# Performance work log

Measured on AMD Instinct MI355X. Metric: run time of the kernel, lower is better.

The kernel has to match this reference:

```python
import jax, jax.numpy as jnp
import numpy as np

B, IN, OUT = 8192, 4096, 4096

def setup_inputs() -> dict:
    key = jax.random.key(0)
    k1, k2, k3 = jax.random.split(key, 3)
    x = jax.random.normal(k1, (B, IN), dtype=jnp.float32)
    # nn.Linear default init: U(-1/sqrt(in), 1/sqrt(in))
    bound = 1.0 / np.sqrt(IN)
    W = jax.random.uniform(k2, (OUT, IN), dtype=jnp.float32, minval=-bound, maxval=bound)
    b = jax.random.uniform(k3, (OUT,), dtype=jnp.float32, minval=-bound, maxval=bound)
    return {"x": x, "W": W, "b": b}

def reference(x, W, b):
    # L2-normalize each row (eps added to norm, matching torch)
    norm = jnp.sqrt(jnp.sum(x * x, axis=1, keepdims=True))
    x_n = x / (norm + 1e-8)
    # Linear: y = x_n @ W^T + b, then ReLU
    y = jnp.einsum('bi,oi->bo', x_n, W) + b
    return jax.nn.relu(y)
```

## Files before the change

### kernel.cpp

```cpp
#include <hip/hip_runtime.h>
#include <hip/hip_bf16.h>
#include <cstdint>
#include <cstddef>

#define GLB(p)  ((const __attribute__((address_space(1))) void*)(p))
#define LDSP(p) ((__attribute__((address_space(3))) void*)(p))

typedef __attribute__((ext_vector_type(8))) __bf16 bf16x8;
typedef __attribute__((ext_vector_type(4))) float  f32x4;
typedef __attribute__((ext_vector_type(8))) unsigned short u16x8;

static constexpr int Mdim = 8192, Ndim = 4096, Kdim = 4096;

#define S_BAR()      do { asm volatile("" ::: "memory"); __builtin_amdgcn_s_barrier(); asm volatile("" ::: "memory"); } while (0)
#define WAIT_LGKM(n) asm volatile("s_waitcnt lgkmcnt(" #n ")" ::: "memory")
#define WAIT_VM(n)   asm volatile("s_waitcnt vmcnt(" #n ")" ::: "memory")

static __device__ __forceinline__ unsigned short f2bf_bits(float f) {
    __hip_bfloat16 h = __float2bfloat16(f);
    return __builtin_bit_cast(unsigned short, h);
}

static __device__ __forceinline__ int swz16k(int p) {
    return p ^ (((p >> 7) & 7) << 4);
}

__global__ void __launch_bounds__(256) preproc_kernel(const float* __restrict__ x,
                                                      const float* __restrict__ Wf,
                                                      __hip_bfloat16* __restrict__ xn,
                                                      __hip_bfloat16* __restrict__ Wb)
{
    const int row = blockIdx.x;
    const int t = threadIdx.x;

    const float4* xr = (const float4*)(x + (size_t)row * Kdim);
    float4 v[4];
    float s = 0.f;
#pragma unroll
    for (int i = 0; i < 4; ++i) {
        v[i] = xr[i * 256 + t];
        s += v[i].x * v[i].x + v[i].y * v[i].y + v[i].z * v[i].z + v[i].w * v[i].w;
    }
#pragma unroll
    for (int off = 32; off > 0; off >>= 1) s += __shfl_down(s, off, 64);
    __shared__ float red[4];
    const int lane = t & 63, w = t >> 6;
    if (lane == 0) red[w] = s;
    __syncthreads();
    const float tot = red[0] + red[1] + red[2] + red[3];
    const float inv = 1.f / (sqrtf(tot) + 1e-8f);
    ushort4* xo = (ushort4*)(xn + (size_t)row * Kdim);
#pragma unroll
    for (int i = 0; i < 4; ++i) {
        ushort4 o;
        o.x = f2bf_bits(v[i].x * inv);
        o.y = f2bf_bits(v[i].y * inv);
        o.z = f2bf_bits(v[i].z * inv);
        o.w = f2bf_bits(v[i].w * inv);
        xo[i * 256 + t] = o;
    }

    const size_t idx = (size_t)row * 256 + t;
    const float4* p = (const float4*)Wf + idx * 2;
    const float4 a = p[0], c = p[1];
    u16x8 o;
    o[0] = f2bf_bits(a.x); o[1] = f2bf_bits(a.y);
    o[2] = f2bf_bits(a.z); o[3] = f2bf_bits(a.w);
    o[4] = f2bf_bits(c.x); o[5] = f2bf_bits(c.y);
    o[6] = f2bf_bits(c.z); o[7] = f2bf_bits(c.w);
    *((u16x8*)Wb + idx) = o;
}

__global__ void __launch_bounds__(512, 2) gemm256_8p(
        const __hip_bfloat16* __restrict__ A,
        const __hip_bfloat16* __restrict__ B,
        const float* __restrict__ bias,
        float* __restrict__ out)
{
    constexpr int NT  = Kdim / 64;
    constexpr int NTN = Ndim / 256;
    constexpr int NWG = (Mdim / 256) * NTN;
    extern __shared__ char smem[];

    const int bid = blockIdx.x;
    const int swz = (bid & 7) * (NWG / 8) + (bid >> 3);
    const int m0 = (swz / NTN) * 256;
    const int n0 = (swz % NTN) * 256;

    const int tid  = threadIdx.x;
    const int lane = tid & 63;
    const int w    = tid >> 6;
    const int wm   = w >> 2;
    const int wn   = w & 3;
    const int fr   = lane & 15;
    const int ko2  = (lane >> 4) * 16;
    const int xm   = (lane & 7) << 4;
    const int brow = (wn & 1) * 64;

    const int p0 = tid * 16;
    const int p1 = 8192 + tid * 16;
    const int q0 = swz16k(p0);
    const int q1 = swz16k(p1);
    const int sr0 = q0 >> 7, sc0 = (q0 & 127) >> 1;
    const int sr1 = q1 >> 7, sc1 = (q1 & 127) >> 1;

    const __hip_bfloat16* Ab0 = A + (size_t)(m0 + sr0) * Kdim + sc0;
    const __hip_bfloat16* Ab1 = A + (size_t)(m0 + sr1) * Kdim + sc1;
    const __hip_bfloat16* Bb0 = B + (size_t)(n0 + sr0) * Kdim + sc0;
    const __hip_bfloat16* Bb1 = B + (size_t)(n0 + sr1) * Kdim + sc1;

#define STAGE_A(tt, h) do { \
        char* ld_ = smem + ((2 * (tt) + (h)) & 3) * 16384; \
        __builtin_amdgcn_global_load_lds(GLB(Ab0 + (size_t)(h) * (128 * Kdim) + (tt) * 64), LDSP(ld_ + p0), 16, 0, 0); \
        __builtin_amdgcn_global_load_lds(GLB(Ab1 + (size_t)(h) * (128 * Kdim) + (tt) * 64), LDSP(ld_ + p1), 16, 0, 0); \
    } while (0)
#define STAGE_B(tt, h) do { \
        char* ld_ = smem + 65536 + ((2 * (tt) + (h)) & 3) * 16384; \
        __builtin_amdgcn_global_load_lds(GLB(Bb0 + (size_t)(h) * (128 * Kdim) + (tt) * 64), LDSP(ld_ + p0), 16, 0, 0); \
        __builtin_amdgcn_global_load_lds(GLB(Bb1 + (size_t)(h) * (128 * Kdim) + (tt) * 64), LDSP(ld_ + p1), 16, 0, 0); \
    } while (0)

#define LDS_RD(base, row, kb) (*(const bf16x8*)(smem + ((((base) + (row) * 128 + (kb))) ^ xm)))

#define A_READS(mb) do { \
    _Pragma("unroll") for (int i = 0; i < 2; ++i) { \
        afr[i][0] = LDS_RD(sa, ((mb) + i) * 16 + fr, ko2); \
        afr[i][1] = LDS_RD(sa, ((mb) + i) * 16 + fr, 64 + ko2); } } while (0)

#define MFMA_PHASE(mb) do { \
    __builtin_amdgcn_s_setprio(1); \
    _Pragma("unroll") for (int kk = 0; kk < 2; ++kk) \
    _Pragma("unroll") for (int i = 0; i < 2; ++i) \
    _Pragma("unroll") for (int j = 0; j < 4; ++j) \
        acc[(mb) + i][j] = __builtin_amdgcn_mfma_f32_16x16x32_bf16(afr[i][kk], bfr[j][kk], acc[(mb) + i][j], 0, 0, 0); \
    __builtin_amdgcn_s_setprio(0); } while (0)

    f32x4 acc[8][4];
#pragma unroll
    for (int i = 0; i < 8; ++i)
#pragma unroll
        for (int j = 0; j < 4; ++j) acc[i][j] = (f32x4){0.f, 0.f, 0.f, 0.f};

    bf16x8 afr[2][2], bfr[4][2];

    STAGE_A(0, 0); STAGE_A(0, 1); STAGE_B(0, 0); STAGE_B(0, 1);
    STAGE_A(1, 0); STAGE_A(1, 1);
    WAIT_VM(4);
    S_BAR();

#pragma unroll 2
    for (int t = 0; t < NT; ++t) {
        const int sa = ((2 * t + wm) & 3) * 16384;
        const int sb = 65536 + ((2 * t + (wn >> 1)) & 3) * 16384;
        const int tb = (t + 1) & (NT - 1);
        const int ta = (t + 2) & (NT - 1);

#pragma unroll
        for (int j = 0; j < 4; ++j) {
            bfr[j][0] = LDS_RD(sb, brow + j * 16 + fr, ko2);
            bfr[j][1] = LDS_RD(sb, brow + j * 16 + fr, 64 + ko2);
        }
        A_READS(0);
        STAGE_B(tb, 0); STAGE_B(tb, 1);
        MFMA_PHASE(0);

        A_READS(2);
        MFMA_PHASE(2);

        A_READS(4);
        MFMA_PHASE(4);

        A_READS(6);
        WAIT_LGKM(0);
        S_BAR();
        STAGE_A(ta, 0); STAGE_A(ta, 1);
        MFMA_PHASE(6);
        WAIT_VM(4);
        S_BAR();
    }
    WAIT_VM(0);

#undef STAGE_A
#undef STAGE_B
#undef LDS_RD
#undef A_READS
#undef MFMA_PHASE

    const int cl = lane & 15;
    const int rl = (lane >> 4) * 4;
#pragma unroll
    for (int j = 0; j < 4; ++j) {
        const int col = n0 + wn * 64 + j * 16 + cl;
        const float bv = bias[col];
#pragma unroll
        for (int i = 0; i < 8; ++i) {
            const int row = m0 + wm * 128 + i * 16 + rl;
            float* po = out + (size_t)row * Ndim + col;
#pragma unroll
            for (int q = 0; q < 4; ++q) {
                const float r = acc[i][j][q] + bv;
                po[(size_t)q * Ndim] = r > 0.f ? r : 0.f;
            }
        }
    }
}

__global__ void __launch_bounds__(256) gemm_bias_relu_kernel(
        const __hip_bfloat16* __restrict__ A,
        const __hip_bfloat16* __restrict__ B,
        const float* __restrict__ bias,
        float* __restrict__ out)
{
    constexpr int BM = 128, BN = 128, BK = 32;
    constexpr int NT_N = Ndim / BN;
    constexpr int NWG  = (Mdim / BM) * NT_N;

    __shared__ __bf16 As[BM * BK];
    __shared__ __bf16 Bs[BN * BK];

    const int bid = blockIdx.x;
    const int swz = (bid & 7) * (NWG / 8) + (bid >> 3);
    const int by = swz / NT_N, bx = swz % NT_N;
    const int m0 = by * BM, n0 = bx * BN;

    const int tid  = threadIdx.x;
    const int lane = tid & 63;
    const int w    = tid >> 6;
    const int wm   = w >> 1, wn = w & 1;

    const int o0 = w * 1024 + lane * 16;
    const int o1 = o0 + 4096;
    const int r0 = o0 >> 6, e0 = (o0 & 63) >> 1;
    const int r1 = o1 >> 6, e1 = (o1 & 63) >> 1;

    const __hip_bfloat16* a0 = A + (size_t)(m0 + r0) * Kdim + e0;
    const __hip_bfloat16* a1 = A + (size_t)(m0 + r1) * Kdim + e1;
    const __hip_bfloat16* b0 = B + (size_t)(n0 + r0) * Kdim + e0;
    const __hip_bfloat16* b1 = B + (size_t)(n0 + r1) * Kdim + e1;
    __bf16* lA0 = As + (o0 >> 1);
    __bf16* lA1 = As + (o1 >> 1);
    __bf16* lB0 = Bs + (o0 >> 1);
    __bf16* lB1 = Bs + (o1 >> 1);

    f32x4 acc[4][4];
#pragma unroll
    for (int i = 0; i < 4; ++i)
#pragma unroll
        for (int j = 0; j < 4; ++j) acc[i][j] = (f32x4){0.f, 0.f, 0.f, 0.f};

    const int fr = lane & 15;
    const int ko = (lane >> 4) * 8;

    for (int kt = 0; kt < Kdim; kt += BK) {
        __builtin_amdgcn_global_load_lds(GLB(a0 + kt), LDSP(lA0), 16, 0, 0);
        __builtin_amdgcn_global_load_lds(GLB(a1 + kt), LDSP(lA1), 16, 0, 0);
        __builtin_amdgcn_global_load_lds(GLB(b0 + kt), LDSP(lB0), 16, 0, 0);
        __builtin_amdgcn_global_load_lds(GLB(b1 + kt), LDSP(lB1), 16, 0, 0);
        __syncthreads();

        bf16x8 af[4], bfr[4];
#pragma unroll
        for (int i = 0; i < 4; ++i)
            af[i]  = *(const bf16x8*)&As[(wm * 64 + i * 16 + fr) * BK + ko];
#pragma unroll
        for (int j = 0; j < 4; ++j)
            bfr[j] = *(const bf16x8*)&Bs[(wn * 64 + j * 16 + fr) * BK + ko];

#pragma unroll
        for (int i = 0; i < 4; ++i)
#pragma unroll
            for (int j = 0; j < 4; ++j)
                acc[i][j] = __builtin_amdgcn_mfma_f32_16x16x32_bf16(af[i], bfr[j], acc[i][j], 0, 0, 0);
        __syncthreads();
    }

    const int cl = lane & 15;
    const int rl = (lane >> 4) * 4;
#pragma unroll
    for (int j = 0; j < 4; ++j) {
        const int col = n0 + wn * 64 + j * 16 + cl;
        const float bv = bias[col];
#pragma unroll
        for (int i = 0; i < 4; ++i) {
            const int row = m0 + wm * 64 + i * 16 + rl;
            float* po = out + (size_t)row * Ndim + col;
#pragma unroll
            for (int q = 0; q < 4; ++q) {
                const float r = acc[i][j][q] + bv;
                po[(size_t)q * Ndim] = r > 0.f ? r : 0.f;
            }
        }
    }
}

__global__ void __launch_bounds__(256) rownorm_only_kernel(const float* __restrict__ x,
                                                           float* __restrict__ invn)
{
    const int row = blockIdx.x;
    const int t = threadIdx.x;
    const float4* xr = (const float4*)(x + (size_t)row * Kdim);
    float s = 0.f;
#pragma unroll
    for (int i = 0; i < 4; ++i) {
        const float4 v = xr[i * 256 + t];
        s += v.x * v.x + v.y * v.y + v.z * v.z + v.w * v.w;
    }
#pragma unroll
    for (int off = 32; off > 0; off >>= 1) s += __shfl_down(s, off, 64);
    __shared__ float red[4];
    if ((t & 63) == 0) red[t >> 6] = s;
    __syncthreads();
    if (t == 0) {
        const float tot = red[0] + red[1] + red[2] + red[3];
        invn[row] = 1.f / (sqrtf(tot) + 1e-8f);
    }
}

__global__ void __launch_bounds__(256) fallback_gemm_kernel(
        const float* __restrict__ x, const float* __restrict__ W,
        const float* __restrict__ b, const float* __restrict__ invn,
        float* __restrict__ out)
{
    __shared__ float At[16][17], Bt[16][17];
    const int tx = threadIdx.x & 15, ty = threadIdx.x >> 4;
    const int m = blockIdx.y * 16 + ty;
    const int n = blockIdx.x * 16 + tx;
    float s = 0.f;
    for (int k0 = 0; k0 < Kdim; k0 += 16) {
        At[ty][tx] = x[(size_t)m * Kdim + k0 + tx];
        Bt[ty][tx] = W[(size_t)(blockIdx.x * 16 + ty) * Kdim + k0 + tx];
        __syncthreads();
#pragma unroll
        for (int kk = 0; kk < 16; ++kk) s += At[ty][kk] * Bt[tx][kk];
        __syncthreads();
    }
    s = s * invn[m] + b[n];
    out[(size_t)m * Ndim + n] = s > 0.f ? s : 0.f;
}

extern "C" void kernel_launch(void* const* d_in, const int* in_sizes, int n_in,
                              void* d_out, int out_size, void* d_ws, size_t ws_size,
                              hipStream_t stream)
{
    (void)in_sizes; (void)n_in; (void)out_size;
    const float* x = (const float*)d_in[0];
    const float* W = (const float*)d_in[1];
    const float* b = (const float*)d_in[2];
    float* out = (float*)d_out;

    const size_t needA = (size_t)Mdim * Kdim * sizeof(__hip_bfloat16);
    const size_t needW = (size_t)Ndim * Kdim * sizeof(__hip_bfloat16);

    if (ws_size >= needA + needW) {
        __hip_bfloat16* Xn = (__hip_bfloat16*)d_ws;
        __hip_bfloat16* Wb = (__hip_bfloat16*)((char*)d_ws + needA);
        preproc_kernel<<<Mdim, 256, 0, stream>>>(x, W, Xn, Wb);

        hipError_t e = hipFuncSetAttribute((const void*)gemm256_8p,
                                           hipFuncAttributeMaxDynamicSharedMemorySize,
                                           131072);
        if (e == hipSuccess) {
            gemm256_8p<<<(Mdim / 256) * (Ndim / 256), 512, 131072, stream>>>(Xn, Wb, b, out);
        } else {
            gemm_bias_relu_kernel<<<(Mdim / 128) * (Ndim / 128), 256, 0, stream>>>(Xn, Wb, b, out);
        }
    } else {
        float* invn = (float*)d_ws;
        rownorm_only_kernel<<<Mdim, 256, 0, stream>>>(x, invn);
        dim3 g(Ndim / 16, Mdim / 16);
        fallback_gemm_kernel<<<g, 256, 0, stream>>>(x, W, b, invn, out);
    }
}
```

Measured before the change: 287.3 us.

## Split 256x256 GEMM tile across 16 waves instead of 8

Launches the 256x256 bf16 GEMM tile with 1024 threads (16 waves) so each wave owns a 64x64 subtile, halving per-wave accumulators and the number of global-to-LDS loads issued per thread. The K loop is restructured into two half-K passes with one A fragment at a time and 4 MFMAs per fragment. The intent is more latency hiding through extra waves per CU. In exchange, each A/B fragment read from LDS is reused fewer times per wave, so LDS traffic per MFMA rises, and the 128KB LDS footprint still limits residency to one block per CU.

```diff
diff --git a/kernel.cpp b/kernel.cpp
--- a/kernel.cpp
+++ b/kernel.cpp
@@ -71,7 +71,7 @@
     *((u16x8*)Wb + idx) = o;
 }
 
-__global__ void __launch_bounds__(512, 2) gemm256_8p(
+__global__ void __launch_bounds__(1024, 4) gemm256_16w(
         const __hip_bfloat16* __restrict__ A,
         const __hip_bfloat16* __restrict__ B,
         const float* __restrict__ bias,
@@ -95,87 +95,75 @@
     const int fr   = lane & 15;
     const int ko2  = (lane >> 4) * 16;
     const int xm   = (lane & 7) << 4;
-    const int brow = (wn & 1) * 64;
+    const int arow = (wm & 1) * 64 + fr;
+    const int brow = (wn & 1) * 64 + fr;
 
     const int p0 = tid * 16;
-    const int p1 = 8192 + tid * 16;
     const int q0 = swz16k(p0);
-    const int q1 = swz16k(p1);
     const int sr0 = q0 >> 7, sc0 = (q0 & 127) >> 1;
-    const int sr1 = q1 >> 7, sc1 = (q1 & 127) >> 1;
 
     const __hip_bfloat16* Ab0 = A + (size_t)(m0 + sr0) * Kdim + sc0;
-    const __hip_bfloat16* Ab1 = A + (size_t)(m0 + sr1) * Kdim + sc1;
     const __hip_bfloat16* Bb0 = B + (size_t)(n0 + sr0) * Kdim + sc0;
-    const __hip_bfloat16* Bb1 = B + (size_t)(n0 + sr1) * Kdim + sc1;
 
 #define STAGE_A(tt, h) do { \
         char* ld_ = smem + ((2 * (tt) + (h)) & 3) * 16384; \
         __builtin_amdgcn_global_load_lds(GLB(Ab0 + (size_t)(h) * (128 * Kdim) + (tt) * 64), LDSP(ld_ + p0), 16, 0, 0); \
-        __builtin_amdgcn_global_load_lds(GLB(Ab1 + (size_t)(h) * (128 * Kdim) + (tt) * 64), LDSP(ld_ + p1), 16, 0, 0); \
     } while (0)
 #define STAGE_B(tt, h) do { \
         char* ld_ = smem + 65536 + ((2 * (tt) + (h)) & 3) * 16384; \
         __builtin_amdgcn_global_load_lds(GLB(Bb0 + (size_t)(h) * (128 * Kdim) + (tt) * 64), LDSP(ld_ + p0), 16, 0, 0); \
-        __builtin_amdgcn_global_load_lds(GLB(Bb1 + (size_t)(h) * (128 * Kdim) + (tt) * 64), LDSP(ld_ + p1), 16, 0, 0); \
     } while (0)
 
 #define LDS_RD(base, row, kb) (*(const bf16x8*)(smem + ((((base) + (row) * 128 + (kb))) ^ xm)))
 
-#define A_READS(mb) do { \
-    _Pragma("unroll") for (int i = 0; i < 2; ++i) { \
-        afr[i][0] = LDS_RD(sa, ((mb) + i) * 16 + fr, ko2); \
-        afr[i][1] = LDS_RD(sa, ((mb) + i) * 16 + fr, 64 + ko2); } } while (0)
-
-#define MFMA_PHASE(mb) do { \
+#define MFMA4(m) do { \
     __builtin_amdgcn_s_setprio(1); \
-    _Pragma("unroll") for (int kk = 0; kk < 2; ++kk) \
-    _Pragma("unroll") for (int i = 0; i < 2; ++i) \
     _Pragma("unroll") for (int j = 0; j < 4; ++j) \
-        acc[(mb) + i][j] = __builtin_amdgcn_mfma_f32_16x16x32_bf16(afr[i][kk], bfr[j][kk], acc[(mb) + i][j], 0, 0, 0); \
+        acc[(m)][j] = __builtin_amdgcn_mfma_f32_16x16x32_bf16(afr, bfr[j], acc[(m)][j], 0, 0, 0); \
     __builtin_amdgcn_s_setprio(0); } while (0)
 
-    f32x4 acc[8][4];
-#pragma unroll
-    for (int i = 0; i < 8; ++i)
+    f32x4 acc[4][4];
+#pragma unroll
+    for (int i = 0; i < 4; ++i)
 #pragma unroll
         for (int j = 0; j < 4; ++j) acc[i][j] = (f32x4){0.f, 0.f, 0.f, 0.f};
 
-    bf16x8 afr[2][2], bfr[4][2];
+    bf16x8 afr, bfr[4];
 
     STAGE_A(0, 0); STAGE_A(0, 1); STAGE_B(0, 0); STAGE_B(0, 1);
     STAGE_A(1, 0); STAGE_A(1, 1);
-    WAIT_VM(4);
+    WAIT_VM(2);
     S_BAR();
 
 #pragma unroll 2
     for (int t = 0; t < NT; ++t) {
-        const int sa = ((2 * t + wm) & 3) * 16384;
+        const int sa = ((2 * t + (wm >> 1)) & 3) * 16384;
         const int sb = 65536 + ((2 * t + (wn >> 1)) & 3) * 16384;
         const int tb = (t + 1) & (NT - 1);
         const int ta = (t + 2) & (NT - 1);
 
 #pragma unroll
-        for (int j = 0; j < 4; ++j) {
-            bfr[j][0] = LDS_RD(sb, brow + j * 16 + fr, ko2);
-            bfr[j][1] = LDS_RD(sb, brow + j * 16 + fr, 64 + ko2);
-        }
-        A_READS(0);
+        for (int j = 0; j < 4; ++j) bfr[j] = LDS_RD(sb, brow + j * 16, ko2);
         STAGE_B(tb, 0); STAGE_B(tb, 1);
-        MFMA_PHASE(0);
-
-        A_READS(2);
-        MFMA_PHASE(2);
-
-        A_READS(4);
-        MFMA_PHASE(4);
-
-        A_READS(6);
+#pragma unroll
+        for (int m = 0; m < 4; ++m) {
+            afr = LDS_RD(sa, arow + m * 16, ko2);
+            MFMA4(m);
+        }
+
+#pragma unroll
+        for (int j = 0; j < 4; ++j) bfr[j] = LDS_RD(sb, brow + j * 16, 64 + ko2);
+#pragma unroll
+        for (int m = 0; m < 3; ++m) {
+            afr = LDS_RD(sa, arow + m * 16, 64 + ko2);
+            MFMA4(m);
+        }
+        afr = LDS_RD(sa, arow + 3 * 16, 64 + ko2);
         WAIT_LGKM(0);
         S_BAR();
         STAGE_A(ta, 0); STAGE_A(ta, 1);
-        MFMA_PHASE(6);
-        WAIT_VM(4);
+        MFMA4(3);
+        WAIT_VM(2);
         S_BAR();
     }
     WAIT_VM(0);
@@ -183,8 +171,7 @@
 #undef STAGE_A
 #undef STAGE_B
 #undef LDS_RD
-#undef A_READS
-#undef MFMA_PHASE
+#undef MFMA4
 
     const int cl = lane & 15;
     const int rl = (lane >> 4) * 4;
@@ -193,8 +180,8 @@
         const int col = n0 + wn * 64 + j * 16 + cl;
         const float bv = bias[col];
 #pragma unroll
-        for (int i = 0; i < 8; ++i) {
-            const int row = m0 + wm * 128 + i * 16 + rl;
+        for (int i = 0; i < 4; ++i) {
+            const int row = m0 + wm * 64 + i * 16 + rl;
             float* po = out + (size_t)row * Ndim + col;
 #pragma unroll
             for (int q = 0; q < 4; ++q) {
@@ -356,11 +343,11 @@
         __hip_bfloat16* Wb = (__hip_bfloat16*)((char*)d_ws + needA);
         preproc_kernel<<<Mdim, 256, 0, stream>>>(x, W, Xn, Wb);
 
-        hipError_t e = hipFuncSetAttribute((const void*)gemm256_8p,
+        hipError_t e = hipFuncSetAttribute((const void*)gemm256_16w,
                                            hipFuncAttributeMaxDynamicSharedMemorySize,
                                            131072);
         if (e == hipSuccess) {
-            gemm256_8p<<<(Mdim / 256) * (Ndim / 256), 512, 131072, stream>>>(Xn, Wb, b, out);
+            gemm256_16w<<<(Mdim / 256) * (Ndim / 256), 1024, 131072, stream>>>(Xn, Wb, b, out);
         } else {
             gemm_bias_relu_kernel<<<(Mdim / 128) * (Ndim / 128), 256, 0, stream>>>(Xn, Wb, b, out);
         }
```

Result: slower. 362.8 us (+26.3%).
